# Performance work log

Hardware: AMD Instinct MI355X
Metric: run time of the kernel (lower is better)

The kernel has to match this reference:

```python
import jax, jax.numpy as jnp
import numpy as np

B, S, D, H = 4, 1024, 1024, 16
DK = D // H
NEG = -1e9


def setup_inputs() -> dict:
    key = jax.random.key(0)
    ks = jax.random.split(key, 14)
    sc = 1.0 / np.sqrt(D)
    inp = {
        "query": jax.random.normal(ks[0], (B, S, D), jnp.float32),
        "key": jax.random.normal(ks[1], (B, S, D), jnp.float32),
        "value": jax.random.normal(ks[2], (B, S, D), jnp.float32),
        "mask": jax.random.randint(ks[3], (B, S, S), 0, 2, jnp.int32),
        "group_prob": jax.random.uniform(ks[4], (B, S, S), jnp.float32),
        "Wq": jax.random.normal(ks[5], (D, D), jnp.float32) * sc,
        "bq": jnp.zeros((D,), jnp.float32),
        "Wk": jax.random.normal(ks[6], (D, D), jnp.float32) * sc,
        "bk": jnp.zeros((D,), jnp.float32),
        "Wv": jax.random.normal(ks[7], (D, D), jnp.float32) * sc,
        "bv": jnp.zeros((D,), jnp.float32),
        "Wo": jax.random.normal(ks[8], (D, D), jnp.float32) * sc,
        "bo": jnp.zeros((D,), jnp.float32),
    }
    return inp


def reference(query, key, value, mask, group_prob, Wq, bq, Wk, bk, Wv, bv, Wo, bo):
    # QKV projections, split heads: [B,S,D] -> [B,H,S,DK]
    def proj(x, W, b):
        return (x @ W.T + b).reshape(B, S, H, DK).transpose(0, 2, 1, 3)

    q = proj(query, Wq, bq)
    k = proj(key, Wk, bk)
    v = proj(value, Wv, bv)

    scores = jnp.einsum("bhqd,bhkd->bhqk", q, k) / jnp.sqrt(jnp.float32(DK))

    # group_prob branch: allowed where mask OR diagonal is nonzero
    diag = jnp.eye(S, dtype=jnp.int32)
    allowed = (mask[:, None, :, :] | diag[None, None, :, :]) != 0  # [B,1,S,S]
    scores = jnp.where(allowed, scores, NEG)

    p_attn = jax.nn.softmax(scores, axis=-1)
    p_attn = p_attn * group_prob[:, None, :, :]  # post-softmax group reweighting

    x = jnp.einsum("bhqk,bhkd->bhqd", p_attn, v)
    x = x.transpose(0, 2, 1, 3).reshape(B, S, D)
    return x @ Wo.T + bo
```

## Files before the change

kernel.cpp:

```cpp
#include <hip/hip_runtime.h>
#include <hip/hip_bf16.h>


#define AS1q __attribute__((address_space(1)))
#define AS3q __attribute__((address_space(3)))

typedef __attribute__((ext_vector_type(8))) __bf16 bf16x8;
typedef __attribute__((ext_vector_type(4))) float f32x4;
typedef __attribute__((ext_vector_type(8))) unsigned short u16x8;

#define GSTR 40

__device__ __forceinline__ void gload_lds16(const void* g, void* l) {
  __builtin_amdgcn_global_load_lds((const AS1q void*)g, (AS3q void*)l, 16, 0, 0);
}
__device__ __forceinline__ bf16x8 lds_read8(const unsigned short* p) {
  bf16x8 r;
  __builtin_memcpy(&r, __builtin_assume_aligned(p, 16), 16);
  return r;
}
__device__ __forceinline__ void lds_write8(unsigned short* p, const void* v) {
  __builtin_memcpy(__builtin_assume_aligned(p, 16), v, 16);
}
__device__ __forceinline__ u16x8 cvt8h(const float4 a, const float4 b) {
  const float fv[8] = {a.x, a.y, a.z, a.w, b.x, b.y, b.z, b.w};
  union { u16x8 v; __bf16 e[8]; } hh;
#pragma unroll
  for (int i = 0; i < 8; ++i) hh.e[i] = (__bf16)fv[i];
  return hh.v;
}
__device__ __forceinline__ void cvt8hl(const float4 a, const float4 b, u16x8* hi, u16x8* lo) {
  const float fv[8] = {a.x, a.y, a.z, a.w, b.x, b.y, b.z, b.w};
  union { u16x8 v; __bf16 e[8]; } hh, ll;
#pragma unroll
  for (int i = 0; i < 8; ++i) {
    const __bf16 h = (__bf16)fv[i];
    hh.e[i] = h;
    ll.e[i] = (__bf16)(fv[i] - (float)h);
  }
  *hi = hh.v; *lo = ll.v;
}
__device__ __forceinline__ unsigned short bfbits(float f) {
  const __bf16 h = (__bf16)f;
  unsigned short u; __builtin_memcpy(&u, &h, 2); return u;
}

__global__ __launch_bounds__(256) void k_prep(
    const int* __restrict__ Mask, const float* __restrict__ Gp, float* __restrict__ G2)
{
  const size_t f = (size_t)blockIdx.x * 256 + threadIdx.x;
  const size_t e = f << 2;
  const int k0 = (int)(e & 1023), q = (int)((e >> 10) & 1023);
  const int4 m4 = *(const int4*)(Mask + e);
  const float4 g4 = *(const float4*)(Gp + e);
  float4 r;
  r.x = (m4.x | (q == k0 + 0)) ? g4.x : -1.f;
  r.y = (m4.y | (q == k0 + 1)) ? g4.y : -1.f;
  r.z = (m4.z | (q == k0 + 2)) ? g4.z : -1.f;
  r.w = (m4.w | (q == k0 + 3)) ? g4.w : -1.f;
  *(float4*)(G2 + e) = r;
}

__global__ __launch_bounds__(256) void k_gemm_qkv(
    const float* __restrict__ X0, const float* __restrict__ X1, const float* __restrict__ X2,
    const float* __restrict__ W0, const float* __restrict__ W1, const float* __restrict__ W2,
    const float* __restrict__ B0, const float* __restrict__ B1, const float* __restrict__ B2,
    unsigned short* __restrict__ O0, unsigned short* __restrict__ O1,
    unsigned short* __restrict__ O2)
{
  const int z = blockIdx.z;
  const float* X = (z == 0) ? X0 : (z == 1) ? X1 : X2;
  const float* W = (z == 0) ? W0 : (z == 1) ? W1 : W2;
  const float* Bi = (z == 0) ? B0 : (z == 1) ? B1 : B2;
  unsigned short* O = (z == 0) ? O0 : (z == 1) ? O1 : O2;

  const int bid = blockIdx.x;
  const int swz = (bid & 7) * 64 + (bid >> 3);
  const int n0 = (swz & 15) * 64, m0 = (swz >> 4) * 128;

  __shared__ alignas(16) unsigned short Ah[128 * GSTR];
  __shared__ alignas(16) unsigned short Bh[64 * GSTR];
  const int tid = threadIdx.x, l = tid & 63, w = tid >> 6;
  const int wr = w >> 1, wc = w & 1;

  f32x4 acc[4][2];
#pragma unroll
  for (int i = 0; i < 4; ++i)
#pragma unroll
    for (int j = 0; j < 2; ++j) acc[i][j] = (f32x4){0.f, 0.f, 0.f, 0.f};

  const int arow = tid >> 1, ac0 = (tid & 1) * 16;
  const int brow = tid >> 2, bc0 = (tid & 3) * 8;
  const float* xsrc = X + (size_t)(m0 + arow) * 1024 + ac0;
  const float* wsrc = W + (size_t)(n0 + brow) * 1024 + bc0;

  float4 fx[4], fw[2];
#pragma unroll
  for (int i = 0; i < 4; ++i) fx[i] = *(const float4*)(xsrc + i * 4);
#pragma unroll
  for (int i = 0; i < 2; ++i) fw[i] = *(const float4*)(wsrc + i * 4);

  for (int kt = 0; kt < 32; ++kt) {
    u16x8 xh[2], wh1;
    xh[0] = cvt8h(fx[0], fx[1]);
    xh[1] = cvt8h(fx[2], fx[3]);
    wh1 = cvt8h(fw[0], fw[1]);
    if (kt < 31) {
      const float* nx = xsrc + (kt + 1) * 32;
      const float* nw = wsrc + (kt + 1) * 32;
#pragma unroll
      for (int i = 0; i < 4; ++i) fx[i] = *(const float4*)(nx + i * 4);
#pragma unroll
      for (int i = 0; i < 2; ++i) fw[i] = *(const float4*)(nw + i * 4);
    }
    __syncthreads();
    lds_write8(&Ah[arow * GSTR + ac0], &xh[0]);
    lds_write8(&Ah[arow * GSTR + ac0 + 8], &xh[1]);
    lds_write8(&Bh[brow * GSTR + bc0], &wh1);
    __syncthreads();

    bf16x8 ah[4], bh[2];
#pragma unroll
    for (int mf = 0; mf < 4; ++mf) {
      const int r = wr * 64 + mf * 16 + (l & 15);
      ah[mf] = lds_read8(&Ah[r * GSTR + (l >> 4) * 8]);
    }
#pragma unroll
    for (int nf = 0; nf < 2; ++nf) {
      const int r = wc * 32 + nf * 16 + (l & 15);
      bh[nf] = lds_read8(&Bh[r * GSTR + (l >> 4) * 8]);
    }
#pragma unroll
    for (int mf = 0; mf < 4; ++mf)
#pragma unroll
      for (int nf = 0; nf < 2; ++nf)
        acc[mf][nf] = __builtin_amdgcn_mfma_f32_16x16x32_bf16(ah[mf], bh[nf], acc[mf][nf], 0, 0, 0);
  }

#pragma unroll
  for (int nf = 0; nf < 2; ++nf) {
    const int col = n0 + wc * 32 + nf * 16 + (l & 15);
    const float bias = Bi[col];
#pragma unroll
    for (int mf = 0; mf < 4; ++mf) {
      const int rbase = m0 + wr * 64 + mf * 16 + (l >> 4) * 4;
#pragma unroll
      for (int j = 0; j < 4; ++j)
        O[(size_t)(rbase + j) * 1024 + col] = bfbits(acc[mf][nf][j] + bias);
    }
  }
}

__global__ __launch_bounds__(256) void k_gemm_out(
    const unsigned short* __restrict__ X, const float* __restrict__ W,
    const float* __restrict__ Bi, float* __restrict__ Out)
{
  const int bid = blockIdx.x;
  const int swz = (bid & 7) * 128 + (bid >> 3);
  const int n0 = (swz & 15) * 64, m0 = (swz >> 4) * 64;

  __shared__ alignas(16) unsigned short Ah[64 * GSTR];
  __shared__ alignas(16) unsigned short Bh[64 * GSTR], Bl[64 * GSTR];
  const int tid = threadIdx.x, l = tid & 63, w = tid >> 6;
  const int wr = w >> 1, wc = w & 1;

  f32x4 acc[2][2];
#pragma unroll
  for (int i = 0; i < 2; ++i)
#pragma unroll
    for (int j = 0; j < 2; ++j) acc[i][j] = (f32x4){0.f, 0.f, 0.f, 0.f};

  const int srow = tid >> 2, sc0 = (tid & 3) * 8;
  const unsigned short* xsrc = X + (size_t)(m0 + srow) * 1024 + sc0;
  const float* wsrc = W + (size_t)(n0 + srow) * 1024 + sc0;

  u16x8 xcur = *(const u16x8*)xsrc;
  float4 fw[2];
#pragma unroll
  for (int i = 0; i < 2; ++i) fw[i] = *(const float4*)(wsrc + i * 4);

  for (int kt = 0; kt < 32; ++kt) {
    const u16x8 xstage = xcur;
    u16x8 wh1, wl1;
    cvt8hl(fw[0], fw[1], &wh1, &wl1);
    if (kt < 31) {
      xcur = *(const u16x8*)(xsrc + (kt + 1) * 32);
      const float* nw = wsrc + (kt + 1) * 32;
#pragma unroll
      for (int i = 0; i < 2; ++i) fw[i] = *(const float4*)(nw + i * 4);
    }
    __syncthreads();
    lds_write8(&Ah[srow * GSTR + sc0], &xstage);
    lds_write8(&Bh[srow * GSTR + sc0], &wh1);
    lds_write8(&Bl[srow * GSTR + sc0], &wl1);
    __syncthreads();

    bf16x8 ah[2], bh[2], bl[2];
#pragma unroll
    for (int mf = 0; mf < 2; ++mf) {
      const int r = wr * 32 + mf * 16 + (l & 15);
      ah[mf] = lds_read8(&Ah[r * GSTR + (l >> 4) * 8]);
    }
#pragma unroll
    for (int nf = 0; nf < 2; ++nf) {
      const int r = wc * 32 + nf * 16 + (l & 15);
      bh[nf] = lds_read8(&Bh[r * GSTR + (l >> 4) * 8]);
      bl[nf] = lds_read8(&Bl[r * GSTR + (l >> 4) * 8]);
    }
#pragma unroll
    for (int mf = 0; mf < 2; ++mf)
#pragma unroll
      for (int nf = 0; nf < 2; ++nf) {
        acc[mf][nf] = __builtin_amdgcn_mfma_f32_16x16x32_bf16(ah[mf], bh[nf], acc[mf][nf], 0, 0, 0);
        acc[mf][nf] = __builtin_amdgcn_mfma_f32_16x16x32_bf16(ah[mf], bl[nf], acc[mf][nf], 0, 0, 0);
      }
  }

#pragma unroll
  for (int nf = 0; nf < 2; ++nf) {
    const int col = n0 + wc * 32 + nf * 16 + (l & 15);
    const float bias = Bi[col];
#pragma unroll
    for (int mf = 0; mf < 2; ++mf) {
      const int rbase = m0 + wr * 32 + mf * 16 + (l >> 4) * 4;
#pragma unroll
      for (int j = 0; j < 4; ++j)
        Out[(size_t)(rbase + j) * 1024 + col] = acc[mf][nf][j] + bias;
    }
  }
}

__global__ __launch_bounds__(256) void k_attn(
    const unsigned short* Qh, const unsigned short* __restrict__ Kb,
    const unsigned short* __restrict__ Vb,
    const float* __restrict__ G2, unsigned short* Xo)
{
  const int i = blockIdx.x;
  const int xc = i & 7, kk_ = i >> 3;
  const int h = kk_ & 15, g = kk_ >> 4;
  const int qb = g * 8 + xc;
  const int qt = qb >> 2, b = qb & 3;

  __shared__ alignas(16) unsigned short Kh[2][64 * 64];
  __shared__ alignas(16) unsigned short Vh[64 * 64];
  __shared__ alignas(16) unsigned short Ph[64 * 64];
  const int tid = threadIdx.x, l = tid & 63, w = tid >> 6;

  const unsigned short* kb_ = Kb + (size_t)b * 1048576 + h * 64;
  const unsigned short* vb_ = Vb + (size_t)b * 1048576 + h * 64;

  bf16x8 aq[2];
  {
    const int qrow = qt * 64 + w * 16 + (l & 15);
    const unsigned short* qp_ = Qh + ((size_t)(b * 1024 + qrow)) * 1024 + h * 64;
    aq[0] = lds_read8(qp_ + (l >> 4) * 8);
    aq[1] = lds_read8(qp_ + 32 + (l >> 4) * 8);
  }

  f32x4 accO[4];
#pragma unroll
  for (int nf = 0; nf < 4; ++nf) accO[nf] = (f32x4){0.f, 0.f, 0.f, 0.f};
  float zacc[4] = {0.f, 0.f, 0.f, 0.f};

  const int qloc0 = w * 16 + (l >> 4) * 4;
  const int qg0 = qt * 64 + qloc0;
  const int mcol = l & 15;

  const float* grow[4];
#pragma unroll
  for (int j = 0; j < 4; ++j)
    grow[j] = G2 + (((size_t)(b * 1024 + qg0 + j)) << 10) + mcol;

  const int srcg8 = ((l & 7) ^ (l >> 3)) * 8;
  const int rowl = l >> 3;
  const int kb4 = (tid & 15) * 4, db4 = (tid >> 4) * 4;
  union U4 { unsigned int u[2]; unsigned short s[4]; };
  U4 vr[4];

#pragma unroll
  for (int I = 0; I < 2; ++I)
    gload_lds16(kb_ + (size_t)(I * 32 + w * 8 + rowl) * 1024 + srcg8,
                &Kh[0][I * 2048 + w * 512]);
#pragma unroll
  for (int ii = 0; ii < 4; ++ii)
    __builtin_memcpy(&vr[ii], vb_ + (size_t)(kb4 + ii) * 1024 + db4, 8);

  float gcur[4][4], gnext[4][4];
#pragma unroll
  for (int nf = 0; nf < 4; ++nf)
#pragma unroll
    for (int j = 0; j < 4; ++j) gcur[nf][j] = grow[j][nf * 16];

  int buf = 0;
  for (int kt = 0; kt < 16; ++kt) {
    __syncthreads();

#pragma unroll
    for (int ii = 0; ii < 4; ++ii) {
      const int d = db4 + ii;
      union { unsigned short s[4]; unsigned long long v; } pk;
#pragma unroll
      for (int u = 0; u < 4; ++u) pk.s[u] = vr[u].s[ii];
      const int c = kb4 ^ ((d & 7) << 3);
      __builtin_memcpy(__builtin_assume_aligned(&Vh[d * 64 + c], 8), &pk.v, 8);
    }
    __syncthreads();

    if (kt < 15) {
#pragma unroll
      for (int I = 0; I < 2; ++I)
        gload_lds16(kb_ + (size_t)((kt + 1) * 64 + I * 32 + w * 8 + rowl) * 1024 + srcg8,
                    &Kh[buf ^ 1][I * 2048 + w * 512]);
#pragma unroll
      for (int ii = 0; ii < 4; ++ii)
        __builtin_memcpy(&vr[ii], vb_ + (size_t)((kt + 1) * 64 + kb4 + ii) * 1024 + db4, 8);
#pragma unroll
      for (int nf = 0; nf < 4; ++nf)
#pragma unroll
        for (int j = 0; j < 4; ++j) gnext[nf][j] = grow[j][(kt + 1) * 64 + nf * 16];
    }

#pragma unroll
    for (int nf = 0; nf < 4; ++nf) {
      f32x4 sacc = (f32x4){0.f, 0.f, 0.f, 0.f};
      const int kr = nf * 16 + (l & 15);
#pragma unroll
      for (int ks = 0; ks < 2; ++ks) {
        const int c = (ks * 32 + (l >> 4) * 8) ^ ((kr & 7) << 3);
        sacc = __builtin_amdgcn_mfma_f32_16x16x32_bf16(aq[ks], lds_read8(&Kh[buf][kr * 64 + c]), sacc, 0, 0, 0);
      }
#pragma unroll
      for (int j = 0; j < 4; ++j) {
        const float g2 = gcur[nf][j];
        const float e = (g2 >= 0.f) ? exp2f(fmaf(sacc[j], 0.18033688f, -17.31234049f)) : 0.f;
        zacc[j] += e;
        const int qloc = qloc0 + j;
        Ph[qloc * 64 + ((nf * 16 + mcol) ^ ((qloc & 7) << 3))] = bfbits(e * g2);
      }
    }
    bf16x8 pah[2];
    {
      const int ar = w * 16 + (l & 15);
#pragma unroll
      for (int ks = 0; ks < 2; ++ks) {
        const int c = (ks * 32 + (l >> 4) * 8) ^ ((ar & 7) << 3);
        pah[ks] = lds_read8(&Ph[ar * 64 + c]);
      }
    }
#pragma unroll
    for (int nf = 0; nf < 4; ++nf) {
      const int dr = nf * 16 + (l & 15);
#pragma unroll
      for (int ks = 0; ks < 2; ++ks) {
        const int c = (ks * 32 + (l >> 4) * 8) ^ ((dr & 7) << 3);
        accO[nf] = __builtin_amdgcn_mfma_f32_16x16x32_bf16(pah[ks], lds_read8(&Vh[dr * 64 + c]), accO[nf], 0, 0, 0);
      }
    }
    buf ^= 1;
#pragma unroll
    for (int nf = 0; nf < 4; ++nf)
#pragma unroll
      for (int j = 0; j < 4; ++j) gcur[nf][j] = gnext[nf][j];
  }

#pragma unroll
  for (int j = 0; j < 4; ++j) {
#pragma unroll
    for (int off = 1; off < 16; off <<= 1) zacc[j] += __shfl_xor(zacc[j], off, 64);
  }
  float rz[4];
#pragma unroll
  for (int j = 0; j < 4; ++j) rz[j] = 1.f / zacc[j];

#pragma unroll
  for (int nf = 0; nf < 4; ++nf) {
    const int d = nf * 16 + (l & 15);
#pragma unroll
    for (int j = 0; j < 4; ++j) {
      const int qg = qg0 + j;
      Xo[((size_t)(b * 1024 + qg)) * 1024 + h * 64 + d] = bfbits(accO[nf][j] * rz[j]);
    }
  }
}

extern "C" void kernel_launch(void* const* d_in, const int* in_sizes, int n_in,
                              void* d_out, int out_size, void* d_ws, size_t ws_size,
                              hipStream_t stream) {
  const float* query = (const float*)d_in[0];
  const float* key_in = (const float*)d_in[1];
  const float* value = (const float*)d_in[2];
  const int* mask = (const int*)d_in[3];
  const float* gp = (const float*)d_in[4];
  const float* Wq = (const float*)d_in[5];
  const float* bq = (const float*)d_in[6];
  const float* Wk = (const float*)d_in[7];
  const float* bk = (const float*)d_in[8];
  const float* Wv = (const float*)d_in[9];
  const float* bv = (const float*)d_in[10];
  const float* Wo = (const float*)d_in[11];
  const float* bo = (const float*)d_in[12];
  float* out = (float*)d_out;

  unsigned short* kp = (unsigned short*)d_ws;
  unsigned short* vp = kp + 4194304;
  unsigned short* qp = vp + 4194304;
  unsigned short* xo = qp;
  float* g2 = (float*)(qp + 4194304);

  hipLaunchKernelGGL(k_prep, dim3(4096), dim3(256), 0, stream, mask, gp, g2);
  hipLaunchKernelGGL(k_gemm_qkv, dim3(512, 1, 3), dim3(256), 0, stream,
                     query, key_in, value, Wq, Wk, Wv, bq, bk, bv, qp, kp, vp);
  hipLaunchKernelGGL(k_attn, dim3(1024), dim3(256), 0, stream,
                     qp, kp, vp, g2, xo);
  hipLaunchKernelGGL(k_gemm_out, dim3(1024), dim3(256), 0, stream,
                     xo, Wo, bo, out);
}
```

Baseline: 186.3 us.

## Pre-convert weights to bf16, store mask-gated group prob as bf16, double-buffer GEMM LDS

Adds a kernel that converts Wq/Wk/Wv to bf16 and splits Wo into bf16 hi/lo once per call, so the GEMMs load half the weight bytes and skip in-loop conversion. The combined mask/group-prob tensor is now stored as bf16 instead of fp32, halving its write and read traffic in the attention kernel. Both GEMMs move to double-buffered LDS with a single barrier per k-step. The costs are an extra kernel launch, more LDS per block, and rounding group_prob to bf16, which lowers precision.

```diff
diff --git a/kernel.cpp b/kernel.cpp
--- a/kernel.cpp
+++ b/kernel.cpp
@@ -22,6 +22,9 @@
 __device__ __forceinline__ void lds_write8(unsigned short* p, const void* v) {
   __builtin_memcpy(__builtin_assume_aligned(p, 16), v, 16);
 }
+__device__ __forceinline__ float bf2f(unsigned short u) {
+  union { unsigned int i; float f; } v; v.i = ((unsigned int)u) << 16; return v.f;
+}
 __device__ __forceinline__ u16x8 cvt8h(const float4 a, const float4 b) {
   const float fv[8] = {a.x, a.y, a.z, a.w, b.x, b.y, b.z, b.w};
   union { u16x8 v; __bf16 e[8]; } hh;
@@ -45,32 +48,61 @@
   unsigned short u; __builtin_memcpy(&u, &h, 2); return u;
 }
 
-__global__ __launch_bounds__(256) void k_prep(
-    const int* __restrict__ Mask, const float* __restrict__ Gp, float* __restrict__ G2)
+__global__ __launch_bounds__(256) void k_prep_g2(
+    const int* __restrict__ Mask, const float* __restrict__ Gp,
+    unsigned short* __restrict__ G2)
 {
-  const size_t f = (size_t)blockIdx.x * 256 + threadIdx.x;
-  const size_t e = f << 2;
+  const size_t e = ((size_t)blockIdx.x * 256 + threadIdx.x) * 8;
   const int k0 = (int)(e & 1023), q = (int)((e >> 10) & 1023);
-  const int4 m4 = *(const int4*)(Mask + e);
-  const float4 g4 = *(const float4*)(Gp + e);
-  float4 r;
-  r.x = (m4.x | (q == k0 + 0)) ? g4.x : -1.f;
-  r.y = (m4.y | (q == k0 + 1)) ? g4.y : -1.f;
-  r.z = (m4.z | (q == k0 + 2)) ? g4.z : -1.f;
-  r.w = (m4.w | (q == k0 + 3)) ? g4.w : -1.f;
-  *(float4*)(G2 + e) = r;
+  const int4 m0 = *(const int4*)(Mask + e);
+  const int4 m1 = *(const int4*)(Mask + e + 4);
+  const float4 g0 = *(const float4*)(Gp + e);
+  const float4 g1 = *(const float4*)(Gp + e + 4);
+  const int mm[8] = {m0.x, m0.y, m0.z, m0.w, m1.x, m1.y, m1.z, m1.w};
+  const float gg[8] = {g0.x, g0.y, g0.z, g0.w, g1.x, g1.y, g1.z, g1.w};
+  union { u16x8 v; unsigned short s[8]; } r;
+#pragma unroll
+  for (int i = 0; i < 8; ++i)
+    r.s[i] = bfbits((mm[i] | (q == k0 + i)) ? gg[i] : -1.f);
+  *(u16x8*)(G2 + e) = r.v;
+}
+
+__global__ __launch_bounds__(256) void k_prep_w(
+    const float* __restrict__ Wq, const float* __restrict__ Wk,
+    const float* __restrict__ Wv, const float* __restrict__ Wo,
+    unsigned short* __restrict__ Qw, unsigned short* __restrict__ Kw,
+    unsigned short* __restrict__ Vw, unsigned short* __restrict__ Oh,
+    unsigned short* __restrict__ Ol)
+{
+  const int z = blockIdx.z;
+  const size_t e = ((size_t)blockIdx.x * 256 + threadIdx.x) * 8;
+  if (z < 3) {
+    const float* S = (z == 0) ? Wq : (z == 1) ? Wk : Wv;
+    unsigned short* D = (z == 0) ? Qw : (z == 1) ? Kw : Vw;
+    const float4 a = *(const float4*)(S + e);
+    const float4 b = *(const float4*)(S + e + 4);
+    *(u16x8*)(D + e) = cvt8h(a, b);
+  } else {
+    const float4 a = *(const float4*)(Wo + e);
+    const float4 b = *(const float4*)(Wo + e + 4);
+    u16x8 hi, lo;
+    cvt8hl(a, b, &hi, &lo);
+    *(u16x8*)(Oh + e) = hi;
+    *(u16x8*)(Ol + e) = lo;
+  }
 }
 
 __global__ __launch_bounds__(256) void k_gemm_qkv(
     const float* __restrict__ X0, const float* __restrict__ X1, const float* __restrict__ X2,
-    const float* __restrict__ W0, const float* __restrict__ W1, const float* __restrict__ W2,
+    const unsigned short* __restrict__ W0, const unsigned short* __restrict__ W1,
+    const unsigned short* __restrict__ W2,
     const float* __restrict__ B0, const float* __restrict__ B1, const float* __restrict__ B2,
     unsigned short* __restrict__ O0, unsigned short* __restrict__ O1,
     unsigned short* __restrict__ O2)
 {
   const int z = blockIdx.z;
   const float* X = (z == 0) ? X0 : (z == 1) ? X1 : X2;
-  const float* W = (z == 0) ? W0 : (z == 1) ? W1 : W2;
+  const unsigned short* W = (z == 0) ? W0 : (z == 1) ? W1 : W2;
   const float* Bi = (z == 0) ? B0 : (z == 1) ? B1 : B2;
   unsigned short* O = (z == 0) ? O0 : (z == 1) ? O1 : O2;
 
@@ -78,8 +110,8 @@
   const int swz = (bid & 7) * 64 + (bid >> 3);
   const int n0 = (swz & 15) * 64, m0 = (swz >> 4) * 128;
 
-  __shared__ alignas(16) unsigned short Ah[128 * GSTR];
-  __shared__ alignas(16) unsigned short Bh[64 * GSTR];
+  __shared__ alignas(16) unsigned short Ah[2][128 * GSTR];
+  __shared__ alignas(16) unsigned short Bh[2][64 * GSTR];
   const int tid = threadIdx.x, l = tid & 63, w = tid >> 6;
   const int wr = w >> 1, wc = w & 1;
 
@@ -92,49 +124,55 @@
   const int arow = tid >> 1, ac0 = (tid & 1) * 16;
   const int brow = tid >> 2, bc0 = (tid & 3) * 8;
   const float* xsrc = X + (size_t)(m0 + arow) * 1024 + ac0;
-  const float* wsrc = W + (size_t)(n0 + brow) * 1024 + bc0;
-
-  float4 fx[4], fw[2];
+  const unsigned short* wsrc = W + (size_t)(n0 + brow) * 1024 + bc0;
+
+  float4 fx[4];
+  u16x8 bx;
 #pragma unroll
   for (int i = 0; i < 4; ++i) fx[i] = *(const float4*)(xsrc + i * 4);
-#pragma unroll
-  for (int i = 0; i < 2; ++i) fw[i] = *(const float4*)(wsrc + i * 4);
-
+  bx = *(const u16x8*)(wsrc);
+  {
+    const u16x8 a0 = cvt8h(fx[0], fx[1]), a1 = cvt8h(fx[2], fx[3]);
+    lds_write8(&Ah[0][arow * GSTR + ac0], &a0);
+    lds_write8(&Ah[0][arow * GSTR + ac0 + 8], &a1);
+    lds_write8(&Bh[0][brow * GSTR + bc0], &bx);
+  }
+#pragma unroll
+  for (int i = 0; i < 4; ++i) fx[i] = *(const float4*)(xsrc + 32 + i * 4);
+  bx = *(const u16x8*)(wsrc + 32);
+
+  int buf = 0;
   for (int kt = 0; kt < 32; ++kt) {
-    u16x8 xh[2], wh1;
-    xh[0] = cvt8h(fx[0], fx[1]);
-    xh[1] = cvt8h(fx[2], fx[3]);
-    wh1 = cvt8h(fw[0], fw[1]);
+    __syncthreads();
     if (kt < 31) {
-      const float* nx = xsrc + (kt + 1) * 32;
-      const float* nw = wsrc + (kt + 1) * 32;
-#pragma unroll
-      for (int i = 0; i < 4; ++i) fx[i] = *(const float4*)(nx + i * 4);
-#pragma unroll
-      for (int i = 0; i < 2; ++i) fw[i] = *(const float4*)(nw + i * 4);
-    }
-    __syncthreads();
-    lds_write8(&Ah[arow * GSTR + ac0], &xh[0]);
-    lds_write8(&Ah[arow * GSTR + ac0 + 8], &xh[1]);
-    lds_write8(&Bh[brow * GSTR + bc0], &wh1);
-    __syncthreads();
-
+      const u16x8 a0 = cvt8h(fx[0], fx[1]), a1 = cvt8h(fx[2], fx[3]);
+      lds_write8(&Ah[buf ^ 1][arow * GSTR + ac0], &a0);
+      lds_write8(&Ah[buf ^ 1][arow * GSTR + ac0 + 8], &a1);
+      lds_write8(&Bh[buf ^ 1][brow * GSTR + bc0], &bx);
+      if (kt < 30) {
+        const float* nx = xsrc + (kt + 2) * 32;
+#pragma unroll
+        for (int i = 0; i < 4; ++i) fx[i] = *(const float4*)(nx + i * 4);
+        bx = *(const u16x8*)(wsrc + (kt + 2) * 32);
+      }
+    }
     bf16x8 ah[4], bh[2];
 #pragma unroll
     for (int mf = 0; mf < 4; ++mf) {
       const int r = wr * 64 + mf * 16 + (l & 15);
-      ah[mf] = lds_read8(&Ah[r * GSTR + (l >> 4) * 8]);
+      ah[mf] = lds_read8(&Ah[buf][r * GSTR + (l >> 4) * 8]);
     }
 #pragma unroll
     for (int nf = 0; nf < 2; ++nf) {
       const int r = wc * 32 + nf * 16 + (l & 15);
-      bh[nf] = lds_read8(&Bh[r * GSTR + (l >> 4) * 8]);
+      bh[nf] = lds_read8(&Bh[buf][r * GSTR + (l >> 4) * 8]);
     }
 #pragma unroll
     for (int mf = 0; mf < 4; ++mf)
 #pragma unroll
       for (int nf = 0; nf < 2; ++nf)
         acc[mf][nf] = __builtin_amdgcn_mfma_f32_16x16x32_bf16(ah[mf], bh[nf], acc[mf][nf], 0, 0, 0);
+    buf ^= 1;
   }
 
 #pragma unroll
@@ -152,15 +190,16 @@
 }
 
 __global__ __launch_bounds__(256) void k_gemm_out(
-    const unsigned short* __restrict__ X, const float* __restrict__ W,
-    const float* __restrict__ Bi, float* __restrict__ Out)
+    const unsigned short* __restrict__ X, const unsigned short* __restrict__ Wh,
+    const unsigned short* __restrict__ Wl, const float* __restrict__ Bi,
+    float* __restrict__ Out)
 {
   const int bid = blockIdx.x;
   const int swz = (bid & 7) * 128 + (bid >> 3);
   const int n0 = (swz & 15) * 64, m0 = (swz >> 4) * 64;
 
-  __shared__ alignas(16) unsigned short Ah[64 * GSTR];
-  __shared__ alignas(16) unsigned short Bh[64 * GSTR], Bl[64 * GSTR];
+  __shared__ alignas(16) unsigned short Ah[2][64 * GSTR];
+  __shared__ alignas(16) unsigned short Bh[2][64 * GSTR], Bl[2][64 * GSTR];
   const int tid = threadIdx.x, l = tid & 63, w = tid >> 6;
   const int wr = w >> 1, wc = w & 1;
 
@@ -172,40 +211,41 @@
 
   const int srow = tid >> 2, sc0 = (tid & 3) * 8;
   const unsigned short* xsrc = X + (size_t)(m0 + srow) * 1024 + sc0;
-  const float* wsrc = W + (size_t)(n0 + srow) * 1024 + sc0;
-
-  u16x8 xcur = *(const u16x8*)xsrc;
-  float4 fw[2];
-#pragma unroll
-  for (int i = 0; i < 2; ++i) fw[i] = *(const float4*)(wsrc + i * 4);
-
+  const unsigned short* whs = Wh + (size_t)(n0 + srow) * 1024 + sc0;
+  const unsigned short* wls = Wl + (size_t)(n0 + srow) * 1024 + sc0;
+
+  u16x8 xa = *(const u16x8*)xsrc, wa = *(const u16x8*)whs, la = *(const u16x8*)wls;
+  lds_write8(&Ah[0][srow * GSTR + sc0], &xa);
+  lds_write8(&Bh[0][srow * GSTR + sc0], &wa);
+  lds_write8(&Bl[0][srow * GSTR + sc0], &la);
+  xa = *(const u16x8*)(xsrc + 32);
+  wa = *(const u16x8*)(whs + 32);
+  la = *(const u16x8*)(wls + 32);
+
+  int buf = 0;
   for (int kt = 0; kt < 32; ++kt) {
-    const u16x8 xstage = xcur;
-    u16x8 wh1, wl1;
-    cvt8hl(fw[0], fw[1], &wh1, &wl1);
+    __syncthreads();
     if (kt < 31) {
-      xcur = *(const u16x8*)(xsrc + (kt + 1) * 32);
-      const float* nw = wsrc + (kt + 1) * 32;
-#pragma unroll
-      for (int i = 0; i < 2; ++i) fw[i] = *(const float4*)(nw + i * 4);
-    }
-    __syncthreads();
-    lds_write8(&Ah[srow * GSTR + sc0], &xstage);
-    lds_write8(&Bh[srow * GSTR + sc0], &wh1);
-    lds_write8(&Bl[srow * GSTR + sc0], &wl1);
-    __syncthreads();
-
+      lds_write8(&Ah[buf ^ 1][srow * GSTR + sc0], &xa);
+      lds_write8(&Bh[buf ^ 1][srow * GSTR + sc0], &wa);
+      lds_write8(&Bl[buf ^ 1][srow * GSTR + sc0], &la);
+      if (kt < 30) {
+        xa = *(const u16x8*)(xsrc + (kt + 2) * 32);
+        wa = *(const u16x8*)(whs + (kt + 2) * 32);
+        la = *(const u16x8*)(wls + (kt + 2) * 32);
+      }
+    }
     bf16x8 ah[2], bh[2], bl[2];
 #pragma unroll
     for (int mf = 0; mf < 2; ++mf) {
       const int r = wr * 32 + mf * 16 + (l & 15);
-      ah[mf] = lds_read8(&Ah[r * GSTR + (l >> 4) * 8]);
+      ah[mf] = lds_read8(&Ah[buf][r * GSTR + (l >> 4) * 8]);
     }
 #pragma unroll
     for (int nf = 0; nf < 2; ++nf) {
       const int r = wc * 32 + nf * 16 + (l & 15);
-      bh[nf] = lds_read8(&Bh[r * GSTR + (l >> 4) * 8]);
-      bl[nf] = lds_read8(&Bl[r * GSTR + (l >> 4) * 8]);
+      bh[nf] = lds_read8(&Bh[buf][r * GSTR + (l >> 4) * 8]);
+      bl[nf] = lds_read8(&Bl[buf][r * GSTR + (l >> 4) * 8]);
     }
 #pragma unroll
     for (int mf = 0; mf < 2; ++mf)
@@ -214,6 +254,7 @@
         acc[mf][nf] = __builtin_amdgcn_mfma_f32_16x16x32_bf16(ah[mf], bh[nf], acc[mf][nf], 0, 0, 0);
         acc[mf][nf] = __builtin_amdgcn_mfma_f32_16x16x32_bf16(ah[mf], bl[nf], acc[mf][nf], 0, 0, 0);
       }
+    buf ^= 1;
   }
 
 #pragma unroll
@@ -233,7 +274,7 @@
 __global__ __launch_bounds__(256) void k_attn(
     const unsigned short* Qh, const unsigned short* __restrict__ Kb,
     const unsigned short* __restrict__ Vb,
-    const float* __restrict__ G2, unsigned short* Xo)
+    const unsigned short* __restrict__ G2, unsigned short* Xo)
 {
   const int i = blockIdx.x;
   const int xc = i & 7, kk_ = i >> 3;
@@ -266,7 +307,7 @@
   const int qg0 = qt * 64 + qloc0;
   const int mcol = l & 15;
 
-  const float* grow[4];
+  const unsigned short* grow[4];
 #pragma unroll
   for (int j = 0; j < 4; ++j)
     grow[j] = G2 + (((size_t)(b * 1024 + qg0 + j)) << 10) + mcol;
@@ -289,7 +330,7 @@
 #pragma unroll
   for (int nf = 0; nf < 4; ++nf)
 #pragma unroll
-    for (int j = 0; j < 4; ++j) gcur[nf][j] = grow[j][nf * 16];
+    for (int j = 0; j < 4; ++j) gcur[nf][j] = bf2f(grow[j][nf * 16]);
 
   int buf = 0;
   for (int kt = 0; kt < 16; ++kt) {
@@ -317,7 +358,7 @@
 #pragma unroll
       for (int nf = 0; nf < 4; ++nf)
 #pragma unroll
-        for (int j = 0; j < 4; ++j) gnext[nf][j] = grow[j][(kt + 1) * 64 + nf * 16];
+        for (int j = 0; j < 4; ++j) gnext[nf][j] = bf2f(grow[j][(kt + 1) * 64 + nf * 16]);
     }
 
 #pragma unroll
@@ -405,13 +446,20 @@
   unsigned short* vp = kp + 4194304;
   unsigned short* qp = vp + 4194304;
   unsigned short* xo = qp;
-  float* g2 = (float*)(qp + 4194304);
-
-  hipLaunchKernelGGL(k_prep, dim3(4096), dim3(256), 0, stream, mask, gp, g2);
+  unsigned short* g2 = qp + 4194304;
+  unsigned short* wq = g2 + 4194304;
+  unsigned short* wk = wq + 1048576;
+  unsigned short* wv = wk + 1048576;
+  unsigned short* woh = wv + 1048576;
+  unsigned short* wol = woh + 1048576;
+
+  hipLaunchKernelGGL(k_prep_g2, dim3(2048), dim3(256), 0, stream, mask, gp, g2);
+  hipLaunchKernelGGL(k_prep_w, dim3(512, 1, 4), dim3(256), 0, stream,
+                     Wq, Wk, Wv, Wo, wq, wk, wv, woh, wol);
   hipLaunchKernelGGL(k_gemm_qkv, dim3(512, 1, 3), dim3(256), 0, stream,
-                     query, key_in, value, Wq, Wk, Wv, bq, bk, bv, qp, kp, vp);
+                     query, key_in, value, wq, wk, wv, bq, bk, bv, qp, kp, vp);
   hipLaunchKernelGGL(k_attn, dim3(1024), dim3(256), 0, stream,
                      qp, kp, vp, g2, xo);
   hipLaunchKernelGGL(k_gemm_out, dim3(1024), dim3(256), 0, stream,
-                     xo, Wo, bo, out);
-}
+                     xo, woh, wol, bo, out);
+}
```

Result: slower. 201.4 us (+8.1%).
